# Kernel tuning notes

Measured on AMD Instinct MI355X. Metric: run time of the kernel, lower is better.

## Reference

```python
import math
import jax, jax.numpy as jnp
import numpy as np

EMB = 1024
HEADS = 16
HD = EMB // HEADS  # 64
MAXPOS = 1024
BATCH = 4
SEQ = 1024


def get_rope_cache(dim, max_pos, theta=10000.0):
    # NOTE: faithfully reproduces the (i - 1) quirk of the source (not the standard i)
    i = jnp.arange(dim // 2, dtype=jnp.float32)
    theta_i = theta ** (-2.0 * (i - 1.0) / dim)
    pos = jnp.arange(max_pos, dtype=jnp.float32)[:, None]
    th = pos * theta_i  # [max_pos, dim//2]
    return jnp.stack([jnp.cos(th), jnp.sin(th)], axis=-1)  # [max_pos, dim//2, 2]


def apply_rope(x, rope_cache):
    # x: [B, H, S, hd]. Source casts pairs to float16 before the complex multiply,
    # then the complex32*complex64 product promotes back to float32 -> emulate via
    # an fp16 round-trip on x, with the rotation itself done in fp32.
    B, H, S, hd = x.shape
    rc = rope_cache[:S]  # [S, hd//2, 2]
    xp = x.reshape(B, H, S, hd // 2, 2).astype(jnp.float16).astype(jnp.float32)
    a, b = xp[..., 0], xp[..., 1]
    cos, sin = rc[..., 0], rc[..., 1]
    rot = jnp.stack([a * cos - b * sin, a * sin + b * cos], axis=-1)
    return rot.reshape(B, H, S, hd)


def setup_inputs() -> dict:
    key = jax.random.key(0)
    ks = jax.random.split(key, 5)
    std = math.sqrt(2.0 / (EMB + EMB))
    x = jax.random.normal(ks[0], (BATCH, SEQ, EMB), dtype=jnp.float32)
    padding_mask = jnp.ones((BATCH, SEQ), dtype=jnp.float32)
    Wq = jax.random.normal(ks[1], (EMB, EMB), dtype=jnp.float32) * std
    Wk = jax.random.normal(ks[2], (EMB, EMB), dtype=jnp.float32) * std
    Wv = jax.random.normal(ks[3], (EMB, EMB), dtype=jnp.float32) * std
    Wo = jax.random.normal(ks[4], (EMB, EMB), dtype=jnp.float32) * std
    rope_cache = get_rope_cache(HD, MAXPOS)
    return {"x": x, "padding_mask": padding_mask, "Wq": Wq, "Wk": Wk,
            "Wv": Wv, "Wo": Wo, "rope_cache": rope_cache}


def reference(x, padding_mask, Wq, Wk, Wv, Wo, rope_cache):
    B, S, E = x.shape

    def heads(t):  # [B,S,E] -> [B,H,S,hd]
        return t.reshape(B, S, HEADS, HD).transpose(0, 2, 1, 3)

    q = heads(x @ Wq.T)
    k = heads(x @ Wk.T)
    v = heads(x @ Wv.T)
    q = apply_rope(q, rope_cache)
    k = apply_rope(k, rope_cache)

    scores = jnp.einsum('bhqd,bhkd->bhqk', q, k)  # [B,H,S,S]
    causal = jnp.tril(jnp.ones((S, S), jnp.float32))
    mask = (causal[None, :, :] * padding_mask[:, None, :])[:, None]  # [B,1,S,S]
    scores = jnp.where(mask == 0, jnp.float32(-1e9), scores) / math.sqrt(HD)
    weights = jax.nn.softmax(scores, axis=-1)

    out = jnp.einsum('bhqk,bhkd->bhqd', weights, v)  # [B,H,S,hd]
    # Faithful to source: transpose(-2,-1) then .view(B,S,-1) scrambles head_dim/seq
    out = out.transpose(0, 1, 3, 2).reshape(B, S, E)
    return out @ Wo.T
```

## Files before the change

### kernel.cpp

```cpp
#include <hip/hip_runtime.h>

#define SEQ   1024
#define HEADS 16
#define HD    64
#define BATCH 4
#define EMB   1024

typedef __attribute__((ext_vector_type(8))) short  short8;
typedef __attribute__((ext_vector_type(4))) float  floatx4;

__device__ __forceinline__ unsigned short f2bf(float f) {
    unsigned u = __builtin_bit_cast(unsigned, f);
    u += 0x7FFF + ((u >> 16) & 1);
    return (unsigned short)(u >> 16);
}

__device__ __forceinline__ void g2l16(const void* g, void* l) {
    __builtin_amdgcn_global_load_lds((const __attribute__((address_space(1))) unsigned int*)g,
                                     (__attribute__((address_space(3))) unsigned int*)l,
                                     16, 0, 0);
}

__device__ __forceinline__ short8 ldsfrag(const unsigned short* base, int row, int cq) {
    int ch = cq ^ (row & 7);
    return *(const short8*)(base + row * 64 + ch * 8);
}

__global__ __launch_bounds__(256) void cvt_kernel(
    const float* __restrict__ x,  const float* __restrict__ wq,
    const float* __restrict__ wk, const float* __restrict__ wv,
    const float* __restrict__ wo,
    unsigned short* __restrict__ xb,  unsigned short* __restrict__ wqb,
    unsigned short* __restrict__ wkb, unsigned short* __restrict__ wvb,
    unsigned short* __restrict__ wob) {
    int blk = blockIdx.x;
    const float* src; unsigned short* dst; int rel;
    if      (blk < 4096) { src = x;  dst = xb;  rel = blk; }
    else if (blk < 5120) { src = wq; dst = wqb; rel = blk - 4096; }
    else if (blk < 6144) { src = wk; dst = wkb; rel = blk - 5120; }
    else if (blk < 7168) { src = wv; dst = wvb; rel = blk - 6144; }
    else                 { src = wo; dst = wob; rel = blk - 7168; }
    size_t i = (size_t)rel * 1024 + threadIdx.x * 4;
    float4 v = *(const float4*)(src + i);
    ushort4 o;
    o.x = f2bf(v.x); o.y = f2bf(v.y); o.z = f2bf(v.z); o.w = f2bf(v.w);
    *(ushort4*)(dst + i) = o;
}

template<int MODE>
__global__ __launch_bounds__(256) void gemm_m97(
    const unsigned short* __restrict__ A, const unsigned short* __restrict__ W,
    void* __restrict__ out0, void* __restrict__ out1, void* __restrict__ out2,
    const float* __restrict__ rc, int M, int N, int K) {
    __shared__ unsigned short As[128 * 64];
    __shared__ unsigned short Bs[128 * 64];
    const int tid  = threadIdx.x;
    const int lane = tid & 63;
    const int wid  = tid >> 6;
    const int l15  = lane & 15, quad = lane >> 4;
    const int wm   = (wid & 1) * 64, wn = (wid >> 1) * 64;
    const int m0   = blockIdx.y * 128, n0 = blockIdx.x * 128;
    const int boff = tid * 16;

    floatx4 acc[4][4] = {};
    const char* Ab = (const char*)A;
    const char* Wb = (const char*)W;
    const size_t rstride = (size_t)K * 2;

    for (int k0 = 0; k0 < K; k0 += 64) {
#pragma unroll
        for (int c = 0; c < 4; c++) {
            int o = c * 4096 + boff;
            int row = o >> 7;
            int sw  = ((o >> 4) & 7) ^ (row & 7);
            g2l16(Ab + (size_t)(m0 + row) * rstride + (size_t)k0 * 2 + sw * 16, (char*)As + o);
            g2l16(Wb + (size_t)(n0 + row) * rstride + (size_t)k0 * 2 + sw * 16, (char*)Bs + o);
        }
        __syncthreads();
#pragma unroll
        for (int ks = 0; ks < 2; ks++) {
            short8 a[4], b[4];
#pragma unroll
            for (int i = 0; i < 4; i++) a[i] = ldsfrag(As, wm + i * 16 + l15, ks * 4 + quad);
#pragma unroll
            for (int j = 0; j < 4; j++) b[j] = ldsfrag(Bs, wn + j * 16 + l15, ks * 4 + quad);
#pragma unroll
            for (int i = 0; i < 4; i++)
#pragma unroll
                for (int j = 0; j < 4; j++)
                    acc[i][j] = __builtin_amdgcn_mfma_f32_16x16x32_bf16(a[i], b[j], acc[i][j], 0, 0, 0);
        }
        __syncthreads();
    }

    const int which = n0 >> 10;
#pragma unroll
    for (int i = 0; i < 4; i++) {
#pragma unroll
        for (int r = 0; r < 4; r++) {
            int m = m0 + wm + i * 16 + quad * 4 + r;
            int bb = m >> 10, s = m & 1023;
#pragma unroll
            for (int j = 0; j < 4; j++) {
                int n = n0 + wn + j * 16 + l15;
                float v = acc[i][j][r];
                if (MODE == 0) {
                    ((float*)out0)[(size_t)m * N + n] = v;
                } else {
                    int nr = n & 1023, h = nr >> 6, d = nr & 63;
                    if (which < 2) {
                        float vp = __shfl_xor(v, 1);
                        float2 cs = *(const float2*)&rc[(size_t)s * 64 + (d & ~1)];
                        v = (l15 & 1) ? (vp * cs.y + v * cs.x) : (v * cs.x - vp * cs.y);
                        unsigned short* dst = (which == 0) ? (unsigned short*)out0
                                                           : (unsigned short*)out1;
                        dst[(((size_t)bb * HEADS + h) * SEQ + s) * HD + d] = f2bf(v);
                    } else {
                        ((unsigned short*)out2)[(((size_t)bb * HEADS + h) * HD + d) * SEQ + s] = f2bf(v);
                    }
                }
            }
        }
    }
}

__global__ __launch_bounds__(256) void attn_kernel(
    const unsigned short* __restrict__ Qb, const unsigned short* __restrict__ Kb,
    const unsigned short* __restrict__ VTb, const float* __restrict__ pm,
    unsigned short* __restrict__ Tb) {
    __shared__ unsigned short Ks[64 * 64];
    __shared__ unsigned short Vs[64 * 64];
    __shared__ unsigned short Ps[4][16][72];
    __shared__ float pmf[64];
    const int tid  = threadIdx.x;
    const int lane = tid & 63, wid = tid >> 6;
    const int l15  = lane & 15, quad = lane >> 4;
    const int bh   = blockIdx.x, b = bh >> 4;
    const int q0   = (15 - blockIdx.y) * 64;
    const int qw   = q0 + wid * 16;
    const int q    = qw + l15;
    const unsigned short* Qh  = Qb  + (size_t)bh * SEQ * HD;
    const unsigned short* Kh  = Kb  + (size_t)bh * SEQ * HD;
    const unsigned short* VTh = VTb + (size_t)bh * HD * SEQ;
    unsigned short*       Th  = Tb  + (size_t)bh * HD * SEQ;
    const float* pmb = pm + b * SEQ;
    const float SCL2 = 0.125f * 1.44269504088896340736f;

    short8 qf0 = *(const short8*)&Qh[(size_t)q * HD + quad * 8];
    short8 qf1 = *(const short8*)&Qh[(size_t)q * HD + 32 + quad * 8];

    floatx4 ot[4] = {};
    float l_lane = 0.f;
    unsigned short (*Pw)[72] = Ps[wid];
    const int boff = tid * 16;

    for (int kvc = 0; kvc <= q0; kvc += 64) {
        const char* kg = (const char*)(Kh + (size_t)kvc * HD);
        const char* vg = (const char*)(VTh + kvc);
#pragma unroll
        for (int c = 0; c < 2; c++) {
            int o = c * 4096 + boff;
            int row = o >> 7;
            int sw  = ((o >> 4) & 7) ^ (row & 7);
            g2l16(kg + (size_t)row * 128 + sw * 16, (char*)Ks + o);
            g2l16(vg + (size_t)row * (SEQ * 2) + sw * 16, (char*)Vs + o);
        }
        if (tid < 64) pmf[tid] = (pmb[kvc + tid] != 0.f) ? 1.f : 0.f;
        __syncthreads();

        const bool diag = (kvc + 63 > qw);
        floatx4 sc[4];
#pragma unroll
        for (int st = 0; st < 4; st++) {
            short8 ka0 = ldsfrag(Ks, st * 16 + l15, quad);
            short8 ka1 = ldsfrag(Ks, st * 16 + l15, 4 + quad);
            floatx4 z = {0.f, 0.f, 0.f, 0.f};
            z = __builtin_amdgcn_mfma_f32_16x16x32_bf16(ka0, qf0, z, 0, 0, 0);
            z = __builtin_amdgcn_mfma_f32_16x16x32_bf16(ka1, qf1, z, 0, 0, 0);
            sc[st] = z;
        }
#pragma unroll
        for (int st = 0; st < 4; st++) {
            float4 pmv = *(const float4*)&pmf[st * 16 + quad * 4];
            int kvbase = kvc + st * 16 + quad * 4;
            ushort4 pk;
#pragma unroll
            for (int r = 0; r < 4; r++) {
                float e = exp2f(sc[st][r] * SCL2) * ((&pmv.x)[r]);
                if (diag && (kvbase + r > q)) e = 0.f;
                l_lane += e;
                (&pk.x)[r] = f2bf(e);
            }
            *(ushort4*)&Pw[l15][st * 16 + quad * 4] = pk;
        }
        asm volatile("s_waitcnt lgkmcnt(0)" ::: "memory");
        short8 pf0 = *(const short8*)&Pw[l15][quad * 8];
        short8 pf1 = *(const short8*)&Pw[l15][32 + quad * 8];

#pragma unroll
        for (int jt = 0; jt < 4; jt++) {
            short8 v0 = ldsfrag(Vs, jt * 16 + l15, quad);
            short8 v1 = ldsfrag(Vs, jt * 16 + l15, 4 + quad);
            ot[jt] = __builtin_amdgcn_mfma_f32_16x16x32_bf16(v0, pf0, ot[jt], 0, 0, 0);
            ot[jt] = __builtin_amdgcn_mfma_f32_16x16x32_bf16(v1, pf1, ot[jt], 0, 0, 0);
        }
        __syncthreads();
    }

    float l = l_lane;
    l += __shfl_xor(l, 16);
    l += __shfl_xor(l, 32);
    float inv = 1.0f / l;
#pragma unroll
    for (int jt = 0; jt < 4; jt++)
#pragma unroll
        for (int r = 0; r < 4; r++)
            Th[(size_t)(jt * 16 + quad * 4 + r) * SEQ + q] = f2bf(ot[jt][r] * inv);
}

extern "C" void kernel_launch(void* const* d_in, const int* in_sizes, int n_in,
                              void* d_out, int out_size, void* d_ws, size_t ws_size,
                              hipStream_t stream) {
    const float* x  = (const float*)d_in[0];
    const float* pm = (const float*)d_in[1];
    const float* Wq = (const float*)d_in[2];
    const float* Wk = (const float*)d_in[3];
    const float* Wv = (const float*)d_in[4];
    const float* Wo = (const float*)d_in[5];
    const float* rc = (const float*)d_in[6];

    char* base = (char*)d_ws;
    unsigned short* xb   = (unsigned short*)(base);
    unsigned short* wqkv = (unsigned short*)(base + (8u  << 20));
    unsigned short* wob  = (unsigned short*)(base + (14u << 20));
    unsigned short* Qb   = (unsigned short*)(base + (16u << 20));
    unsigned short* Kb   = (unsigned short*)(base + (24u << 20));
    unsigned short* VTb  = (unsigned short*)(base + (32u << 20));
    unsigned short* Tb   = (unsigned short*)(base + (40u << 20));

    cvt_kernel<<<8192, 256, 0, stream>>>(x, Wq, Wk, Wv, Wo,
                                         xb, wqkv, wqkv + (1u << 20), wqkv + (2u << 20), wob);
    gemm_m97<1><<<dim3(24, 32), 256, 0, stream>>>(xb, wqkv, (void*)Qb, (void*)Kb, (void*)VTb,
                                                  rc, 4096, 3072, 1024);
    attn_kernel<<<dim3(64, 16), 256, 0, stream>>>(Qb, Kb, VTb, pm, Tb);
    gemm_m97<0><<<dim3(8, 32), 256, 0, stream>>>(Tb, wob, d_out, nullptr, nullptr,
                                                 nullptr, 4096, 1024, 1024);
}
```

Measured before the change: 183.4 us.

## Double-buffer K in attention, load V directly to registers, add 64-row output GEMM

The attention kernel now double-buffers K tiles in LDS and prefetches the next tile while computing the current one. V fragments are loaded straight from global memory into registers, and the padding-mask values are read from global instead of being staged through LDS. The output projection moves from the generic GEMM to a new kernel with 64x128 tiles, which doubles the grid to 512 blocks for better CU occupancy. The risks are uncoalesced global V loads and no software pipelining in the new GEMM.

```diff
diff --git a/kernel.cpp b/kernel.cpp
--- a/kernel.cpp
+++ b/kernel.cpp
@@ -124,14 +124,76 @@
     }
 }
 
+__global__ __launch_bounds__(256) void gemm_proj64(
+    const unsigned short* __restrict__ A, const unsigned short* __restrict__ W,
+    float* __restrict__ out, int M, int N, int K) {
+    __shared__ unsigned short As[64 * 64];
+    __shared__ unsigned short Bs[128 * 64];
+    const int tid  = threadIdx.x;
+    const int lane = tid & 63;
+    const int wid  = tid >> 6;
+    const int l15  = lane & 15, quad = lane >> 4;
+    const int wm   = (wid & 1) * 32, wn = (wid >> 1) * 64;
+    const int m0   = blockIdx.y * 64, n0 = blockIdx.x * 128;
+    const int boff = tid * 16;
+
+    floatx4 acc[2][4] = {};
+    const char* Ab = (const char*)A;
+    const char* Wb = (const char*)W;
+    const size_t rstride = (size_t)K * 2;
+
+    for (int k0 = 0; k0 < K; k0 += 64) {
+#pragma unroll
+        for (int c = 0; c < 2; c++) {
+            int o = c * 4096 + boff;
+            int row = o >> 7;
+            int sw  = ((o >> 4) & 7) ^ (row & 7);
+            g2l16(Ab + (size_t)(m0 + row) * rstride + (size_t)k0 * 2 + sw * 16, (char*)As + o);
+        }
+#pragma unroll
+        for (int c = 0; c < 4; c++) {
+            int o = c * 4096 + boff;
+            int row = o >> 7;
+            int sw  = ((o >> 4) & 7) ^ (row & 7);
+            g2l16(Wb + (size_t)(n0 + row) * rstride + (size_t)k0 * 2 + sw * 16, (char*)Bs + o);
+        }
+        __syncthreads();
+#pragma unroll
+        for (int ks = 0; ks < 2; ks++) {
+            short8 a[2], b[4];
+#pragma unroll
+            for (int i = 0; i < 2; i++) a[i] = ldsfrag(As, wm + i * 16 + l15, ks * 4 + quad);
+#pragma unroll
+            for (int j = 0; j < 4; j++) b[j] = ldsfrag(Bs, wn + j * 16 + l15, ks * 4 + quad);
+#pragma unroll
+            for (int i = 0; i < 2; i++)
+#pragma unroll
+                for (int j = 0; j < 4; j++)
+                    acc[i][j] = __builtin_amdgcn_mfma_f32_16x16x32_bf16(a[i], b[j], acc[i][j], 0, 0, 0);
+        }
+        __syncthreads();
+    }
+
+#pragma unroll
+    for (int i = 0; i < 2; i++) {
+#pragma unroll
+        for (int r = 0; r < 4; r++) {
+            int m = m0 + wm + i * 16 + quad * 4 + r;
+#pragma unroll
+            for (int j = 0; j < 4; j++) {
+                int n = n0 + wn + j * 16 + l15;
+                out[(size_t)m * N + n] = acc[i][j][r];
+            }
+        }
+    }
+}
+
 __global__ __launch_bounds__(256) void attn_kernel(
     const unsigned short* __restrict__ Qb, const unsigned short* __restrict__ Kb,
     const unsigned short* __restrict__ VTb, const float* __restrict__ pm,
     unsigned short* __restrict__ Tb) {
-    __shared__ unsigned short Ks[64 * 64];
-    __shared__ unsigned short Vs[64 * 64];
+    __shared__ unsigned short Ks[2][64 * 64];
     __shared__ unsigned short Ps[4][16][72];
-    __shared__ float pmf[64];
     const int tid  = threadIdx.x;
     const int lane = tid & 63, wid = tid >> 6;
     const int l15  = lane & 15, quad = lane >> 4;
@@ -154,26 +216,40 @@
     unsigned short (*Pw)[72] = Ps[wid];
     const int boff = tid * 16;
 
-    for (int kvc = 0; kvc <= q0; kvc += 64) {
+    auto stageK = [&](int bufi, int kvc) {
         const char* kg = (const char*)(Kh + (size_t)kvc * HD);
-        const char* vg = (const char*)(VTh + kvc);
 #pragma unroll
         for (int c = 0; c < 2; c++) {
             int o = c * 4096 + boff;
             int row = o >> 7;
             int sw  = ((o >> 4) & 7) ^ (row & 7);
-            g2l16(kg + (size_t)row * 128 + sw * 16, (char*)Ks + o);
-            g2l16(vg + (size_t)row * (SEQ * 2) + sw * 16, (char*)Vs + o);
-        }
-        if (tid < 64) pmf[tid] = (pmb[kvc + tid] != 0.f) ? 1.f : 0.f;
-        __syncthreads();
-
+            g2l16(kg + (size_t)row * 128 + sw * 16, (char*)Ks[bufi] + o);
+        }
+    };
+
+    stageK(0, 0);
+    asm volatile("s_waitcnt vmcnt(0)" ::: "memory");
+    __syncthreads();
+
+    int cur = 0;
+    for (int kvc = 0; kvc <= q0; kvc += 64) {
+        if (kvc + 64 <= q0) stageK(cur ^ 1, kvc + 64);
+
+        short8 v0[4], v1[4];
+#pragma unroll
+        for (int jt = 0; jt < 4; jt++) {
+            const unsigned short* vr = &VTh[(size_t)(jt * 16 + l15) * SEQ + kvc];
+            v0[jt] = *(const short8*)(vr + quad * 8);
+            v1[jt] = *(const short8*)(vr + 32 + quad * 8);
+        }
+
+        const unsigned short* Kc = Ks[cur];
         const bool diag = (kvc + 63 > qw);
         floatx4 sc[4];
 #pragma unroll
         for (int st = 0; st < 4; st++) {
-            short8 ka0 = ldsfrag(Ks, st * 16 + l15, quad);
-            short8 ka1 = ldsfrag(Ks, st * 16 + l15, 4 + quad);
+            short8 ka0 = ldsfrag(Kc, st * 16 + l15, quad);
+            short8 ka1 = ldsfrag(Kc, st * 16 + l15, 4 + quad);
             floatx4 z = {0.f, 0.f, 0.f, 0.f};
             z = __builtin_amdgcn_mfma_f32_16x16x32_bf16(ka0, qf0, z, 0, 0, 0);
             z = __builtin_amdgcn_mfma_f32_16x16x32_bf16(ka1, qf1, z, 0, 0, 0);
@@ -181,12 +257,12 @@
         }
 #pragma unroll
         for (int st = 0; st < 4; st++) {
-            float4 pmv = *(const float4*)&pmf[st * 16 + quad * 4];
             int kvbase = kvc + st * 16 + quad * 4;
+            float4 pmv = *(const float4*)&pmb[kvbase];
             ushort4 pk;
 #pragma unroll
             for (int r = 0; r < 4; r++) {
-                float e = exp2f(sc[st][r] * SCL2) * ((&pmv.x)[r]);
+                float e = exp2f(sc[st][r] * SCL2) * (((&pmv.x)[r] != 0.f) ? 1.f : 0.f);
                 if (diag && (kvbase + r > q)) e = 0.f;
                 l_lane += e;
                 (&pk.x)[r] = f2bf(e);
@@ -199,12 +275,13 @@
 
 #pragma unroll
         for (int jt = 0; jt < 4; jt++) {
-            short8 v0 = ldsfrag(Vs, jt * 16 + l15, quad);
-            short8 v1 = ldsfrag(Vs, jt * 16 + l15, 4 + quad);
-            ot[jt] = __builtin_amdgcn_mfma_f32_16x16x32_bf16(v0, pf0, ot[jt], 0, 0, 0);
-            ot[jt] = __builtin_amdgcn_mfma_f32_16x16x32_bf16(v1, pf1, ot[jt], 0, 0, 0);
-        }
-        __syncthreads();
+            ot[jt] = __builtin_amdgcn_mfma_f32_16x16x32_bf16(v0[jt], pf0, ot[jt], 0, 0, 0);
+            ot[jt] = __builtin_amdgcn_mfma_f32_16x16x32_bf16(v1[jt], pf1, ot[jt], 0, 0, 0);
+        }
+
+        asm volatile("s_waitcnt vmcnt(0)" ::: "memory");
+        __syncthreads();
+        cur ^= 1;
     }
 
     float l = l_lane;
@@ -243,6 +320,5 @@
     gemm_m97<1><<<dim3(24, 32), 256, 0, stream>>>(xb, wqkv, (void*)Qb, (void*)Kb, (void*)VTb,
                                                   rc, 4096, 3072, 1024);
     attn_kernel<<<dim3(64, 16), 256, 0, stream>>>(Qb, Kb, VTb, pm, Tb);
-    gemm_m97<0><<<dim3(8, 32), 256, 0, stream>>>(Tb, wob, d_out, nullptr, nullptr,
-                                                 nullptr, 4096, 1024, 1024);
-}
+    gemm_proj64<<<dim3(8, 64), 256, 0, stream>>>(Tb, wob, (float*)d_out, 4096, 1024, 1024);
+}
```

Result: slower. 199.3 us (+8.7%).
